# Kernel tuning notes

Hardware: AMD Instinct MI355X
Metric: run time of the kernel (lower is better)

The kernel has to match this reference:

```python
import jax, jax.numpy as jnp
import numpy as np

N = 100000
E = 1600000
IN, HID, OUT = 64, 128, 64
EPS = 1e-5


def _sage_conv(x, src, dst, w_l, b_l, w_r):
    # PyG SAGEConv (mean aggr): out = lin_l(mean_{j in N(i)} x_j) + lin_r(x_i)
    msgs = x[src]                                   # [E, d] gather
    agg = jax.ops.segment_sum(msgs, dst, num_segments=N)  # [N, d]
    deg = jax.ops.segment_sum(jnp.ones((E,), x.dtype), dst, num_segments=N)
    agg = agg / jnp.maximum(deg, 1.0)[:, None]      # mean over neighbors
    return agg @ w_l.T + b_l + x @ w_r.T


def _bn_eval(x, gamma, beta, mean, var):
    return (x - mean) * jax.lax.rsqrt(var + EPS) * gamma + beta


def setup_inputs() -> dict:
    key = jax.random.key(0)
    ks = jax.random.split(key, 16)
    x = jax.random.normal(ks[0], (N, IN), jnp.float32)
    edge_index = jax.random.randint(ks[1], (2, E), 0, N, jnp.int32)
    s1 = 1.0 / np.sqrt(IN)
    s2 = 1.0 / np.sqrt(HID)
    return {
        "x": x,
        "edge_index": edge_index,
        "w1l": jax.random.uniform(ks[2], (HID, IN), jnp.float32, -s1, s1),
        "b1l": jax.random.uniform(ks[3], (HID,), jnp.float32, -s1, s1),
        "w1r": jax.random.uniform(ks[4], (HID, IN), jnp.float32, -s1, s1),
        "bn1_gamma": jax.random.uniform(ks[5], (HID,), jnp.float32, 0.5, 1.5),
        "bn1_beta": jax.random.normal(ks[6], (HID,), jnp.float32) * 0.1,
        "bn1_mean": jax.random.normal(ks[7], (HID,), jnp.float32) * 0.1,
        "bn1_var": jax.random.uniform(ks[8], (HID,), jnp.float32, 0.5, 1.5),
        "w2l": jax.random.uniform(ks[9], (OUT, HID), jnp.float32, -s2, s2),
        "b2l": jax.random.uniform(ks[10], (OUT,), jnp.float32, -s2, s2),
        "w2r": jax.random.uniform(ks[11], (OUT, HID), jnp.float32, -s2, s2),
        "bn2_gamma": jax.random.uniform(ks[12], (OUT,), jnp.float32, 0.5, 1.5),
        "bn2_beta": jax.random.normal(ks[13], (OUT,), jnp.float32) * 0.1,
        "bn2_mean": jax.random.normal(ks[14], (OUT,), jnp.float32) * 0.1,
        "bn2_var": jax.random.uniform(ks[15], (OUT,), jnp.float32, 0.5, 1.5),
    }


def reference(x, edge_index, w1l, b1l, w1r, bn1_gamma, bn1_beta, bn1_mean, bn1_var,
              w2l, b2l, w2r, bn2_gamma, bn2_beta, bn2_mean, bn2_var):
    src, dst = edge_index[0], edge_index[1]
    # layer 1: SAGEConv -> BN -> ReLU (dropout is identity in eval mode)
    h = _sage_conv(x, src, dst, w1l, b1l, w1r)
    h = jax.nn.relu(_bn_eval(h, bn1_gamma, bn1_beta, bn1_mean, bn1_var))
    # layer 2: SAGEConv -> BN
    h = _sage_conv(h, src, dst, w2l, b2l, w2r)
    return _bn_eval(h, bn2_gamma, bn2_beta, bn2_mean, bn2_var)
```

## Files before the change

kernel.cpp:

```cpp
#include <hip/hip_runtime.h>

#define NN 100000
#define NE 1600000
#define EPSV 1e-5f

#define NBUK 196
#define TILE 2048
#define NTIL 782
#define CAP  9216

typedef __attribute__((ext_vector_type(8))) short bf16x8;
typedef __attribute__((ext_vector_type(4))) float f32x4;

__device__ inline unsigned short f2bf(float f) {
  unsigned u = __builtin_bit_cast(unsigned, f);
  unsigned r = u + 0x7FFFu + ((u >> 16) & 1u);
  return (unsigned short)(r >> 16);
}
__device__ inline float bf2f(unsigned short s) {
  unsigned u = ((unsigned)s) << 16;
  return __builtin_bit_cast(float, u);
}

__global__ __launch_bounds__(256) void k_bin(const int* __restrict__ src,
                                             const int* __restrict__ dst,
                                             int* __restrict__ gcur,
                                             unsigned* __restrict__ pairs) {
  __shared__ int cnt[NBUK];
  __shared__ int lo[NBUK];
  __shared__ int gbase[NBUK];
  __shared__ int ts[256];
  __shared__ unsigned stage[TILE];
  const int tid = threadIdx.x;
  const int e0 = blockIdx.x * TILE;
  const int m = min(TILE, NE - e0);

  for (int i = tid; i < NBUK; i += 256) cnt[i] = 0;
  __syncthreads();
  for (int i = tid; i < m; i += 256) {
    int d = dst[e0 + i];
    atomicAdd(&cnt[d >> 9], 1);
  }
  __syncthreads();
  int c = (tid < NBUK) ? cnt[tid] : 0;
  ts[tid] = c;
  __syncthreads();
  for (int d = 1; d < 256; d <<= 1) {
    int v = (tid >= d) ? ts[tid - d] : 0;
    __syncthreads();
    ts[tid] += v;
    __syncthreads();
  }
  if (tid < NBUK) {
    int ex = ts[tid] - c;
    lo[tid] = ex;
    gbase[tid] = atomicAdd(&gcur[tid], c);
    cnt[tid] = ex;
  }
  __syncthreads();
  for (int i = tid; i < m; i += 256) {
    int d = dst[e0 + i];
    int s = src[e0 + i];
    int b = d >> 9;
    int pos = atomicAdd(&cnt[b], 1);
    stage[pos] = ((unsigned)(d & 511) << 17) | (unsigned)s;
  }
  __syncthreads();
  for (int i = tid; i < m; i += 256) {
    int a = 0, z = NBUK - 1;
    while (a < z) {
      int mid = (a + z + 1) >> 1;
      if (lo[mid] <= i) a = mid; else z = mid - 1;
    }
    int rel = gbase[a] + (i - lo[a]);
    if (rel < CAP) pairs[(size_t)a * CAP + rel] = stage[i];
  }
}

__global__ __launch_bounds__(256) void k_bscan(const int* __restrict__ gcur,
                                               int* __restrict__ bucketBase) {
  __shared__ int ts[256];
  const int tid = threadIdx.x;
  int c = (tid < NBUK) ? min(gcur[tid], CAP) : 0;
  ts[tid] = c;
  __syncthreads();
  for (int d = 1; d < 256; d <<= 1) {
    int v = (tid >= d) ? ts[tid - d] : 0;
    __syncthreads();
    ts[tid] += v;
    __syncthreads();
  }
  if (tid < NBUK) bucketBase[tid] = ts[tid] - c;
}

__global__ __launch_bounds__(512) void k_build(const unsigned* __restrict__ pairs,
                                               const int* __restrict__ gcur,
                                               const int* __restrict__ bucketBase,
                                               int* __restrict__ deg,
                                               int* __restrict__ offset,
                                               int* __restrict__ csr) {
  __shared__ int hist[512];
  __shared__ int ts[512];
  __shared__ unsigned stage[CAP];
  const int tid = threadIdx.x;
  const int b = blockIdx.x;
  const int count = min(gcur[b], CAP);
  const int nbase = b * 512;
  const int nloc = min(512, NN - nbase);
  const unsigned* pb = pairs + (size_t)b * CAP;
  const int obase = bucketBase[b];

  hist[tid] = 0;
  __syncthreads();
  for (int i = tid; i < count; i += 512) {
    atomicAdd(&hist[pb[i] >> 17], 1);
  }
  __syncthreads();
  int s = hist[tid];
  ts[tid] = s;
  __syncthreads();
  for (int d = 1; d < 512; d <<= 1) {
    int v = (tid >= d) ? ts[tid - d] : 0;
    __syncthreads();
    ts[tid] += v;
    __syncthreads();
  }
  int ex = ts[tid] - s;
  if (tid < nloc) {
    deg[nbase + tid] = s;
    offset[nbase + tid] = obase + ex;
  }
  __syncthreads();
  hist[tid] = ex;
  __syncthreads();
  for (int i = tid; i < count; i += 512) {
    unsigned e = pb[i];
    int pos = atomicAdd(&hist[e >> 17], 1);
    stage[pos] = e & 0x1FFFFu;
  }
  __syncthreads();
  for (int i = tid; i < count; i += 512) csr[obase + i] = (int)stage[i];
}

__global__ __launch_bounds__(256) void k_wprep(const float* __restrict__ w1l,
                                               const float* __restrict__ w1r,
                                               const float* __restrict__ w2l,
                                               const float* __restrict__ w2r,
                                               const float* __restrict__ b1l,
                                               const float* __restrict__ g1,
                                               const float* __restrict__ be1,
                                               const float* __restrict__ m1,
                                               const float* __restrict__ v1,
                                               const float* __restrict__ b2l,
                                               const float* __restrict__ g2,
                                               const float* __restrict__ be2,
                                               const float* __restrict__ m2,
                                               const float* __restrict__ v2,
                                               unsigned short* __restrict__ w1c,
                                               unsigned short* __restrict__ w2c,
                                               float* __restrict__ bn) {
  int i = blockIdx.x * 256 + threadIdx.x;
  int o = i >> 7, k = i & 127;
  float vv1 = (k < 64) ? w1l[o * 64 + k] : w1r[o * 64 + (k - 64)];
  w1c[i] = f2bf(vv1);
  float vv2 = (o < 64) ? w2l[o * 128 + k] : w2r[(o - 64) * 128 + k];
  w2c[i] = f2bf(vv2);
  if (i < 128) {
    float sc = g1[i] * rsqrtf(v1[i] + EPSV);
    bn[i] = sc;
    bn[128 + i] = (b1l[i] - m1[i]) * sc + be1[i];
  }
  if (i < 64) {
    float sc = g2[i] * rsqrtf(v2[i] + EPSV);
    bn[256 + i] = sc;
    bn[320 + i] = (b2l[i] - m2[i]) * sc + be2[i];
  }
}

__global__ __launch_bounds__(256) void k_cvtx(const float* __restrict__ x,
                                              unsigned short* __restrict__ xb) {
  int i = blockIdx.x * 256 + threadIdx.x;
  float4 v = *(const float4*)(x + (size_t)i * 4);
  ushort4 o;
  o.x = f2bf(v.x); o.y = f2bf(v.y); o.z = f2bf(v.z); o.w = f2bf(v.w);
  *(ushort4*)(xb + (size_t)i * 4) = o;
}

__global__ __launch_bounds__(256) void k_aggregate(const unsigned short* __restrict__ xb,
                                                   const int* __restrict__ deg,
                                                   const int* __restrict__ offset,
                                                   const int* __restrict__ csr,
                                                   unsigned short* __restrict__ aggB) {
  int tid = threadIdx.x;
  int node = blockIdx.x * 32 + (tid >> 3);
  int j = tid & 7;
  int cnt = deg[node];
  const int* arow = csr + offset[node];
  float a0=0.f,a1=0.f,a2=0.f,a3=0.f,a4=0.f,a5=0.f,a6=0.f,a7=0.f;
  int k = 0;
  for (; k + 4 <= cnt; k += 4) {
    int s0 = arow[k], s1 = arow[k+1], s2 = arow[k+2], s3 = arow[k+3];
    uint4 v0 = *(const uint4*)(xb + (size_t)s0 * 64 + j * 8);
    uint4 v1 = *(const uint4*)(xb + (size_t)s1 * 64 + j * 8);
    uint4 v2 = *(const uint4*)(xb + (size_t)s2 * 64 + j * 8);
    uint4 v3 = *(const uint4*)(xb + (size_t)s3 * 64 + j * 8);
    a0 += bf2f(v0.x & 0xffff) + bf2f(v1.x & 0xffff) + bf2f(v2.x & 0xffff) + bf2f(v3.x & 0xffff);
    a1 += bf2f(v0.x >> 16)    + bf2f(v1.x >> 16)    + bf2f(v2.x >> 16)    + bf2f(v3.x >> 16);
    a2 += bf2f(v0.y & 0xffff) + bf2f(v1.y & 0xffff) + bf2f(v2.y & 0xffff) + bf2f(v3.y & 0xffff);
    a3 += bf2f(v0.y >> 16)    + bf2f(v1.y >> 16)    + bf2f(v2.y >> 16)    + bf2f(v3.y >> 16);
    a4 += bf2f(v0.z & 0xffff) + bf2f(v1.z & 0xffff) + bf2f(v2.z & 0xffff) + bf2f(v3.z & 0xffff);
    a5 += bf2f(v0.z >> 16)    + bf2f(v1.z >> 16)    + bf2f(v2.z >> 16)    + bf2f(v3.z >> 16);
    a6 += bf2f(v0.w & 0xffff) + bf2f(v1.w & 0xffff) + bf2f(v2.w & 0xffff) + bf2f(v3.w & 0xffff);
    a7 += bf2f(v0.w >> 16)    + bf2f(v1.w >> 16)    + bf2f(v2.w >> 16)    + bf2f(v3.w >> 16);
  }
  for (; k < cnt; ++k) {
    int s = arow[k];
    uint4 v = *(const uint4*)(xb + (size_t)s * 64 + j * 8);
    a0 += bf2f(v.x & 0xffff); a1 += bf2f(v.x >> 16);
    a2 += bf2f(v.y & 0xffff); a3 += bf2f(v.y >> 16);
    a4 += bf2f(v.z & 0xffff); a5 += bf2f(v.z >> 16);
    a6 += bf2f(v.w & 0xffff); a7 += bf2f(v.w >> 16);
  }
  float inv = 1.0f / fmaxf((float)cnt, 1.0f);
  ushort4 r0, r1;
  r0.x = f2bf(a0 * inv); r0.y = f2bf(a1 * inv); r0.z = f2bf(a2 * inv); r0.w = f2bf(a3 * inv);
  r1.x = f2bf(a4 * inv); r1.y = f2bf(a5 * inv); r1.z = f2bf(a6 * inv); r1.w = f2bf(a7 * inv);
  *(ushort4*)(aggB + (size_t)node * 64 + j * 8) = r0;
  *(ushort4*)(aggB + (size_t)node * 64 + j * 8 + 4) = r1;
}

__global__ __launch_bounds__(256) void k_gemm12(const unsigned short* __restrict__ aggB,
                                                const unsigned short* __restrict__ xb,
                                                const unsigned short* __restrict__ w1c,
                                                const unsigned short* __restrict__ w2c,
                                                const float* __restrict__ bn,
                                                unsigned short* __restrict__ t,
                                                unsigned short* __restrict__ r2) {
  __shared__ unsigned short wlds[32 * 512];
  __shared__ unsigned short hlds[4][2][16 * 128];
  __shared__ float bnlds[384];
  const int tid = threadIdx.x;
  const int w = tid >> 6;
  const int lane = tid & 63;
  const int lr = lane & 15;
  const int q = lane >> 4;
  const int base = blockIdx.x * 128 + w * 32;
  const int nA = base + lr, nB = base + 16 + lr;
  const int cA = min(nA, NN - 1), cB = min(nB, NN - 1);
  const int swz = (lr & 7) << 4;

  bf16x8 fA[4], fB[4];
  {
    const unsigned short* a = aggB + (size_t)cA * 64 + q * 8;
    const unsigned short* xx = xb + (size_t)cA * 64 + q * 8;
    fA[0] = *(const bf16x8*)a;        fA[1] = *(const bf16x8*)(a + 32);
    fA[2] = *(const bf16x8*)xx;       fA[3] = *(const bf16x8*)(xx + 32);
  }
  {
    const unsigned short* a = aggB + (size_t)cB * 64 + q * 8;
    const unsigned short* xx = xb + (size_t)cB * 64 + q * 8;
    fB[0] = *(const bf16x8*)a;        fB[1] = *(const bf16x8*)(a + 32);
    fB[2] = *(const bf16x8*)xx;       fB[3] = *(const bf16x8*)(xx + 32);
  }

  for (int i = tid; i < 384; i += 256) bnlds[i] = bn[i];
  for (int idx = tid; idx < 2048; idx += 256) {
    int f = idx >> 6, l = idx & 63;
    int gofs = ((f >> 2) * 16 + (l & 15)) * 128 + (f & 3) * 32 + (l >> 4) * 8;
    *(uint4*)&wlds[idx * 8] = *(const uint4*)&w1c[gofs];
  }
  __syncthreads();

  char* ldsA = (char*)&hlds[w][0][0];
  char* ldsB = (char*)&hlds[w][1][0];

#pragma unroll
  for (int ot = 0; ot < 8; ++ot) {
    const unsigned short* wp = &wlds[(ot * 4) * 512 + lane * 8];
    bf16x8 w0 = *(const bf16x8*)(wp);
    bf16x8 w1 = *(const bf16x8*)(wp + 512);
    bf16x8 w2 = *(const bf16x8*)(wp + 1024);
    bf16x8 w3 = *(const bf16x8*)(wp + 1536);
    f32x4 aA = {0.f, 0.f, 0.f, 0.f}, aB = {0.f, 0.f, 0.f, 0.f};
    aA = __builtin_amdgcn_mfma_f32_16x16x32_bf16(w0, fA[0], aA, 0, 0, 0);
    aA = __builtin_amdgcn_mfma_f32_16x16x32_bf16(w1, fA[1], aA, 0, 0, 0);
    aA = __builtin_amdgcn_mfma_f32_16x16x32_bf16(w2, fA[2], aA, 0, 0, 0);
    aA = __builtin_amdgcn_mfma_f32_16x16x32_bf16(w3, fA[3], aA, 0, 0, 0);
    aB = __builtin_amdgcn_mfma_f32_16x16x32_bf16(w0, fB[0], aB, 0, 0, 0);
    aB = __builtin_amdgcn_mfma_f32_16x16x32_bf16(w1, fB[1], aB, 0, 0, 0);
    aB = __builtin_amdgcn_mfma_f32_16x16x32_bf16(w2, fB[2], aB, 0, 0, 0);
    aB = __builtin_amdgcn_mfma_f32_16x16x32_bf16(w3, fB[3], aB, 0, 0, 0);
    const int o = ot * 16 + q * 4;
    float4 sc = *(const float4*)&bnlds[o];
    float4 sh = *(const float4*)&bnlds[128 + o];
    ushort4 hA, hB;
    hA.x = f2bf(fmaxf(aA[0] * sc.x + sh.x, 0.f));
    hA.y = f2bf(fmaxf(aA[1] * sc.y + sh.y, 0.f));
    hA.z = f2bf(fmaxf(aA[2] * sc.z + sh.z, 0.f));
    hA.w = f2bf(fmaxf(aA[3] * sc.w + sh.w, 0.f));
    hB.x = f2bf(fmaxf(aB[0] * sc.x + sh.x, 0.f));
    hB.y = f2bf(fmaxf(aB[1] * sc.y + sh.y, 0.f));
    hB.z = f2bf(fmaxf(aB[2] * sc.z + sh.z, 0.f));
    hB.w = f2bf(fmaxf(aB[3] * sc.w + sh.w, 0.f));
    const int wb = lr * 256 + ot * 32 + q * 8;
    *(ushort4*)(ldsA + (wb ^ swz)) = hA;
    *(ushort4*)(ldsB + (wb ^ swz)) = hB;
  }
  __syncthreads();

  for (int idx = tid; idx < 2048; idx += 256) {
    int f = idx >> 6, l = idx & 63;
    int gofs = ((f >> 2) * 16 + (l & 15)) * 128 + (f & 3) * 32 + (l >> 4) * 8;
    *(uint4*)&wlds[idx * 8] = *(const uint4*)&w2c[gofs];
  }
  __syncthreads();

  bf16x8 hA[4], hB[4];
#pragma unroll
  for (int jj = 0; jj < 4; ++jj) {
    const int rb = lr * 256 + jj * 64 + q * 16;
    hA[jj] = *(const bf16x8*)(ldsA + (rb ^ swz));
    hB[jj] = *(const bf16x8*)(ldsB + (rb ^ swz));
  }

#pragma unroll
  for (int ot = 0; ot < 8; ++ot) {
    const unsigned short* wp = &wlds[(ot * 4) * 512 + lane * 8];
    bf16x8 w0 = *(const bf16x8*)(wp);
    bf16x8 w1 = *(const bf16x8*)(wp + 512);
    bf16x8 w2 = *(const bf16x8*)(wp + 1024);
    bf16x8 w3 = *(const bf16x8*)(wp + 1536);
    f32x4 aA = {0.f, 0.f, 0.f, 0.f}, aB = {0.f, 0.f, 0.f, 0.f};
    aA = __builtin_amdgcn_mfma_f32_16x16x32_bf16(w0, hA[0], aA, 0, 0, 0);
    aA = __builtin_amdgcn_mfma_f32_16x16x32_bf16(w1, hA[1], aA, 0, 0, 0);
    aA = __builtin_amdgcn_mfma_f32_16x16x32_bf16(w2, hA[2], aA, 0, 0, 0);
    aA = __builtin_amdgcn_mfma_f32_16x16x32_bf16(w3, hA[3], aA, 0, 0, 0);
    aB = __builtin_amdgcn_mfma_f32_16x16x32_bf16(w0, hB[0], aB, 0, 0, 0);
    aB = __builtin_amdgcn_mfma_f32_16x16x32_bf16(w1, hB[1], aB, 0, 0, 0);
    aB = __builtin_amdgcn_mfma_f32_16x16x32_bf16(w2, hB[2], aB, 0, 0, 0);
    aB = __builtin_amdgcn_mfma_f32_16x16x32_bf16(w3, hB[3], aB, 0, 0, 0);
    ushort4 tv;
    if (ot < 4) {
      const int o = ot * 16 + q * 4;
      tv.x = f2bf(aA[0]); tv.y = f2bf(aA[1]); tv.z = f2bf(aA[2]); tv.w = f2bf(aA[3]);
      if (nA < NN) *(ushort4*)(t + (size_t)nA * 64 + o) = tv;
      tv.x = f2bf(aB[0]); tv.y = f2bf(aB[1]); tv.z = f2bf(aB[2]); tv.w = f2bf(aB[3]);
      if (nB < NN) *(ushort4*)(t + (size_t)nB * 64 + o) = tv;
    } else {
      const int o = (ot - 4) * 16 + q * 4;
      tv.x = f2bf(aA[0]); tv.y = f2bf(aA[1]); tv.z = f2bf(aA[2]); tv.w = f2bf(aA[3]);
      if (nA < NN) *(ushort4*)(r2 + (size_t)nA * 64 + o) = tv;
      tv.x = f2bf(aB[0]); tv.y = f2bf(aB[1]); tv.z = f2bf(aB[2]); tv.w = f2bf(aB[3]);
      if (nB < NN) *(ushort4*)(r2 + (size_t)nB * 64 + o) = tv;
    }
  }
}

__global__ __launch_bounds__(256) void k_agg2fin(const unsigned short* __restrict__ t,
                                                 const int* __restrict__ deg,
                                                 const int* __restrict__ offset,
                                                 const int* __restrict__ csr,
                                                 const unsigned short* __restrict__ r2,
                                                 const float* __restrict__ bn,
                                                 float* __restrict__ outp) {
  int tid = threadIdx.x;
  int node = blockIdx.x * 32 + (tid >> 3);
  int j = tid & 7;
  int cnt = deg[node];
  const int* arow = csr + offset[node];
  float a0=0.f,a1=0.f,a2=0.f,a3=0.f,a4=0.f,a5=0.f,a6=0.f,a7=0.f;
  int k = 0;
  for (; k + 4 <= cnt; k += 4) {
    int s0 = arow[k], s1 = arow[k+1], s2 = arow[k+2], s3 = arow[k+3];
    uint4 v0 = *(const uint4*)(t + (size_t)s0 * 64 + j * 8);
    uint4 v1 = *(const uint4*)(t + (size_t)s1 * 64 + j * 8);
    uint4 v2 = *(const uint4*)(t + (size_t)s2 * 64 + j * 8);
    uint4 v3 = *(const uint4*)(t + (size_t)s3 * 64 + j * 8);
    a0 += bf2f(v0.x & 0xffff) + bf2f(v1.x & 0xffff) + bf2f(v2.x & 0xffff) + bf2f(v3.x & 0xffff);
    a1 += bf2f(v0.x >> 16)    + bf2f(v1.x >> 16)    + bf2f(v2.x >> 16)    + bf2f(v3.x >> 16);
    a2 += bf2f(v0.y & 0xffff) + bf2f(v1.y & 0xffff) + bf2f(v2.y & 0xffff) + bf2f(v3.y & 0xffff);
    a3 += bf2f(v0.y >> 16)    + bf2f(v1.y >> 16)    + bf2f(v2.y >> 16)    + bf2f(v3.y >> 16);
    a4 += bf2f(v0.z & 0xffff) + bf2f(v1.z & 0xffff) + bf2f(v2.z & 0xffff) + bf2f(v3.z & 0xffff);
    a5 += bf2f(v0.z >> 16)    + bf2f(v1.z >> 16)    + bf2f(v2.z >> 16)    + bf2f(v3.z >> 16);
    a6 += bf2f(v0.w & 0xffff) + bf2f(v1.w & 0xffff) + bf2f(v2.w & 0xffff) + bf2f(v3.w & 0xffff);
    a7 += bf2f(v0.w >> 16)    + bf2f(v1.w >> 16)    + bf2f(v2.w >> 16)    + bf2f(v3.w >> 16);
  }
  for (; k < cnt; ++k) {
    int s = arow[k];
    uint4 v = *(const uint4*)(t + (size_t)s * 64 + j * 8);
    a0 += bf2f(v.x & 0xffff); a1 += bf2f(v.x >> 16);
    a2 += bf2f(v.y & 0xffff); a3 += bf2f(v.y >> 16);
    a4 += bf2f(v.z & 0xffff); a5 += bf2f(v.z >> 16);
    a6 += bf2f(v.w & 0xffff); a7 += bf2f(v.w >> 16);
  }
  float inv = 1.0f / fmaxf((float)cnt, 1.0f);
  int o = j * 8;
  uint4 rv = *(const uint4*)(r2 + (size_t)node * 64 + o);
  float r0 = bf2f(rv.x & 0xffff), r1 = bf2f(rv.x >> 16);
  float r2a = bf2f(rv.y & 0xffff), r3 = bf2f(rv.y >> 16);
  float r4 = bf2f(rv.z & 0xffff), r5 = bf2f(rv.z >> 16);
  float r6 = bf2f(rv.w & 0xffff), r7 = bf2f(rv.w >> 16);
  float4 sca = *(const float4*)(bn + 256 + o);
  float4 scb = *(const float4*)(bn + 256 + o + 4);
  float4 sha = *(const float4*)(bn + 320 + o);
  float4 shb = *(const float4*)(bn + 320 + o + 4);
  float4 o0, o1;
  o0.x = (a0 * inv + r0) * sca.x + sha.x;
  o0.y = (a1 * inv + r1) * sca.y + sha.y;
  o0.z = (a2 * inv + r2a) * sca.z + sha.z;
  o0.w = (a3 * inv + r3) * sca.w + sha.w;
  o1.x = (a4 * inv + r4) * scb.x + shb.x;
  o1.y = (a5 * inv + r5) * scb.y + shb.y;
  o1.z = (a6 * inv + r6) * scb.z + shb.z;
  o1.w = (a7 * inv + r7) * scb.w + shb.w;
  *(float4*)(outp + (size_t)node * 64 + o) = o0;
  *(float4*)(outp + (size_t)node * 64 + o + 4) = o1;
}

extern "C" void kernel_launch(void* const* d_in, const int* in_sizes, int n_in,
                              void* d_out, int out_size, void* d_ws, size_t ws_size,
                              hipStream_t stream) {
  const float* x   = (const float*)d_in[0];
  const int*   ei  = (const int*)d_in[1];
  const float* w1l = (const float*)d_in[2];
  const float* b1l = (const float*)d_in[3];
  const float* w1r = (const float*)d_in[4];
  const float* g1  = (const float*)d_in[5];
  const float* be1 = (const float*)d_in[6];
  const float* m1  = (const float*)d_in[7];
  const float* v1  = (const float*)d_in[8];
  const float* w2l = (const float*)d_in[9];
  const float* b2l = (const float*)d_in[10];
  const float* w2r = (const float*)d_in[11];
  const float* g2  = (const float*)d_in[12];
  const float* be2 = (const float*)d_in[13];
  const float* m2  = (const float*)d_in[14];
  const float* v2  = (const float*)d_in[15];
  float* outp = (float*)d_out;

  char* ws = (char*)d_ws;
  int*            gcur       = (int*)ws;
  int*            bucketBase = (int*)(ws + 1024);
  int*            deg        = (int*)(ws + 2048);
  int*            offset     = (int*)(ws + 402048);
  unsigned*       pairs      = (unsigned*)(ws + 802048);
  int*            csr        = (int*)(ws + 8027392);
  unsigned short* w1c        = (unsigned short*)(ws + 14427392);
  unsigned short* w2c        = (unsigned short*)(ws + 14460160);
  float*          bn         = (float*)(ws + 14492928);
  unsigned short* xb         = (unsigned short*)(ws + 14494976);
  unsigned short* aggB       = (unsigned short*)(ws + 27294976);
  unsigned short* t          = (unsigned short*)(ws + 40094976);
  unsigned short* r2         = (unsigned short*)(ws + 52894976);

  const int* srcp = ei;
  const int* dstp = ei + NE;

  hipMemsetAsync(gcur, 0, NBUK * sizeof(int), stream);
  hipLaunchKernelGGL(k_bin, dim3(NTIL), dim3(256), 0, stream,
                     srcp, dstp, gcur, pairs);
  hipLaunchKernelGGL(k_bscan, dim3(1), dim3(256), 0, stream, gcur, bucketBase);
  hipLaunchKernelGGL(k_build, dim3(NBUK), dim3(512), 0, stream,
                     pairs, gcur, bucketBase, deg, offset, csr);
  hipLaunchKernelGGL(k_wprep, dim3(64), dim3(256), 0, stream,
                     w1l, w1r, w2l, w2r, b1l, g1, be1, m1, v1,
                     b2l, g2, be2, m2, v2, w1c, w2c, bn);
  hipLaunchKernelGGL(k_cvtx, dim3(NN * 64 / 1024), dim3(256), 0, stream, x, xb);
  hipLaunchKernelGGL(k_aggregate, dim3(NN / 32), dim3(256), 0, stream,
                     xb, deg, offset, csr, aggB);
  hipLaunchKernelGGL(k_gemm12, dim3((NN + 127) / 128), dim3(256), 0, stream,
                     aggB, xb, w1c, w2c, bn, t, r2);
  hipLaunchKernelGGL(k_agg2fin, dim3(NN / 32), dim3(256), 0, stream,
                     t, deg, offset, csr, r2, bn, outp);
}
```

Before: 150.1 us.

## Fuse layer-1 neighbor aggregation into GEMM kernel and halve CSR bucket size

Removes the separate k_aggregate kernel. Each wave of the GEMM kernel now gathers and averages neighbor features for its 32 nodes and stages the bf16 means in LDS with an XOR swizzle, then feeds them straight to MFMA. This drops the aggB global round trip and one launch. The CSR build also switches to 256-node buckets (391 buckets, smaller capacity), which shortens the per-block scan and LDS staging but doubles the number of blocks in k_build. The halved CAP raises the chance of a bucket overflowing and silently dropping edges.

```diff
diff --git a/kernel.cpp b/kernel.cpp
--- a/kernel.cpp
+++ b/kernel.cpp
@@ -4,10 +4,10 @@
 #define NE 1600000
 #define EPSV 1e-5f
 
-#define NBUK 196
+#define NBUK 391
 #define TILE 2048
 #define NTIL 782
-#define CAP  9216
+#define CAP  4608
 
 typedef __attribute__((ext_vector_type(8))) short bf16x8;
 typedef __attribute__((ext_vector_type(4))) float f32x4;
@@ -39,11 +39,14 @@
   __syncthreads();
   for (int i = tid; i < m; i += 256) {
     int d = dst[e0 + i];
-    atomicAdd(&cnt[d >> 9], 1);
-  }
-  __syncthreads();
-  int c = (tid < NBUK) ? cnt[tid] : 0;
-  ts[tid] = c;
+    atomicAdd(&cnt[d >> 8], 1);
+  }
+  __syncthreads();
+  const int i0 = 2 * tid, i1 = 2 * tid + 1;
+  int c0 = (i0 < NBUK) ? cnt[i0] : 0;
+  int c1 = (i1 < NBUK) ? cnt[i1] : 0;
+  int s2 = c0 + c1;
+  ts[tid] = s2;
   __syncthreads();
   for (int d = 1; d < 256; d <<= 1) {
     int v = (tid >= d) ? ts[tid - d] : 0;
@@ -51,19 +54,19 @@
     ts[tid] += v;
     __syncthreads();
   }
-  if (tid < NBUK) {
-    int ex = ts[tid] - c;
-    lo[tid] = ex;
-    gbase[tid] = atomicAdd(&gcur[tid], c);
-    cnt[tid] = ex;
-  }
+  int ex = ts[tid] - s2;
+  if (i0 < NBUK) { lo[i0] = ex;      gbase[i0] = atomicAdd(&gcur[i0], c0); }
+  if (i1 < NBUK) { lo[i1] = ex + c0; gbase[i1] = atomicAdd(&gcur[i1], c1); }
+  __syncthreads();
+  if (i0 < NBUK) cnt[i0] = lo[i0];
+  if (i1 < NBUK) cnt[i1] = lo[i1];
   __syncthreads();
   for (int i = tid; i < m; i += 256) {
     int d = dst[e0 + i];
     int s = src[e0 + i];
-    int b = d >> 9;
+    int b = d >> 8;
     int pos = atomicAdd(&cnt[b], 1);
-    stage[pos] = ((unsigned)(d & 511) << 17) | (unsigned)s;
+    stage[pos] = ((unsigned)(d & 255) << 17) | (unsigned)s;
   }
   __syncthreads();
   for (int i = tid; i < m; i += 256) {
@@ -81,8 +84,11 @@
                                                int* __restrict__ bucketBase) {
   __shared__ int ts[256];
   const int tid = threadIdx.x;
-  int c = (tid < NBUK) ? min(gcur[tid], CAP) : 0;
-  ts[tid] = c;
+  const int i0 = 2 * tid, i1 = 2 * tid + 1;
+  int c0 = (i0 < NBUK) ? min(gcur[i0], CAP) : 0;
+  int c1 = (i1 < NBUK) ? min(gcur[i1], CAP) : 0;
+  int s2 = c0 + c1;
+  ts[tid] = s2;
   __syncthreads();
   for (int d = 1; d < 256; d <<= 1) {
     int v = (tid >= d) ? ts[tid - d] : 0;
@@ -90,7 +96,9 @@
     ts[tid] += v;
     __syncthreads();
   }
-  if (tid < NBUK) bucketBase[tid] = ts[tid] - c;
+  int ex = ts[tid] - s2;
+  if (i0 < NBUK) bucketBase[i0] = ex;
+  if (i1 < NBUK) bucketBase[i1] = ex + c0;
 }
 
 __global__ __launch_bounds__(512) void k_build(const unsigned* __restrict__ pairs,
@@ -99,39 +107,41 @@
                                                int* __restrict__ deg,
                                                int* __restrict__ offset,
                                                int* __restrict__ csr) {
-  __shared__ int hist[512];
-  __shared__ int ts[512];
+  __shared__ int hist[256];
+  __shared__ int ts[256];
   __shared__ unsigned stage[CAP];
   const int tid = threadIdx.x;
   const int b = blockIdx.x;
   const int count = min(gcur[b], CAP);
-  const int nbase = b * 512;
-  const int nloc = min(512, NN - nbase);
+  const int nbase = b * 256;
+  const int nloc = min(256, NN - nbase);
   const unsigned* pb = pairs + (size_t)b * CAP;
   const int obase = bucketBase[b];
 
-  hist[tid] = 0;
+  if (tid < 256) hist[tid] = 0;
   __syncthreads();
   for (int i = tid; i < count; i += 512) {
     atomicAdd(&hist[pb[i] >> 17], 1);
   }
   __syncthreads();
-  int s = hist[tid];
-  ts[tid] = s;
-  __syncthreads();
-  for (int d = 1; d < 512; d <<= 1) {
-    int v = (tid >= d) ? ts[tid - d] : 0;
-    __syncthreads();
-    ts[tid] += v;
-    __syncthreads();
-  }
-  int ex = ts[tid] - s;
-  if (tid < nloc) {
-    deg[nbase + tid] = s;
-    offset[nbase + tid] = obase + ex;
-  }
-  __syncthreads();
-  hist[tid] = ex;
+  int s = 0;
+  if (tid < 256) { s = hist[tid]; ts[tid] = s; }
+  __syncthreads();
+  for (int d = 1; d < 256; d <<= 1) {
+    int v = 0;
+    if (tid < 256 && tid >= d) v = ts[tid - d];
+    __syncthreads();
+    if (tid < 256) ts[tid] += v;
+    __syncthreads();
+  }
+  if (tid < 256) {
+    int ex = ts[tid] - s;
+    if (tid < nloc) {
+      deg[nbase + tid] = s;
+      offset[nbase + tid] = obase + ex;
+    }
+    hist[tid] = ex;
+  }
   __syncthreads();
   for (int i = tid; i < count; i += 512) {
     unsigned e = pb[i];
@@ -186,51 +196,10 @@
   *(ushort4*)(xb + (size_t)i * 4) = o;
 }
 
-__global__ __launch_bounds__(256) void k_aggregate(const unsigned short* __restrict__ xb,
-                                                   const int* __restrict__ deg,
-                                                   const int* __restrict__ offset,
-                                                   const int* __restrict__ csr,
-                                                   unsigned short* __restrict__ aggB) {
-  int tid = threadIdx.x;
-  int node = blockIdx.x * 32 + (tid >> 3);
-  int j = tid & 7;
-  int cnt = deg[node];
-  const int* arow = csr + offset[node];
-  float a0=0.f,a1=0.f,a2=0.f,a3=0.f,a4=0.f,a5=0.f,a6=0.f,a7=0.f;
-  int k = 0;
-  for (; k + 4 <= cnt; k += 4) {
-    int s0 = arow[k], s1 = arow[k+1], s2 = arow[k+2], s3 = arow[k+3];
-    uint4 v0 = *(const uint4*)(xb + (size_t)s0 * 64 + j * 8);
-    uint4 v1 = *(const uint4*)(xb + (size_t)s1 * 64 + j * 8);
-    uint4 v2 = *(const uint4*)(xb + (size_t)s2 * 64 + j * 8);
-    uint4 v3 = *(const uint4*)(xb + (size_t)s3 * 64 + j * 8);
-    a0 += bf2f(v0.x & 0xffff) + bf2f(v1.x & 0xffff) + bf2f(v2.x & 0xffff) + bf2f(v3.x & 0xffff);
-    a1 += bf2f(v0.x >> 16)    + bf2f(v1.x >> 16)    + bf2f(v2.x >> 16)    + bf2f(v3.x >> 16);
-    a2 += bf2f(v0.y & 0xffff) + bf2f(v1.y & 0xffff) + bf2f(v2.y & 0xffff) + bf2f(v3.y & 0xffff);
-    a3 += bf2f(v0.y >> 16)    + bf2f(v1.y >> 16)    + bf2f(v2.y >> 16)    + bf2f(v3.y >> 16);
-    a4 += bf2f(v0.z & 0xffff) + bf2f(v1.z & 0xffff) + bf2f(v2.z & 0xffff) + bf2f(v3.z & 0xffff);
-    a5 += bf2f(v0.z >> 16)    + bf2f(v1.z >> 16)    + bf2f(v2.z >> 16)    + bf2f(v3.z >> 16);
-    a6 += bf2f(v0.w & 0xffff) + bf2f(v1.w & 0xffff) + bf2f(v2.w & 0xffff) + bf2f(v3.w & 0xffff);
-    a7 += bf2f(v0.w >> 16)    + bf2f(v1.w >> 16)    + bf2f(v2.w >> 16)    + bf2f(v3.w >> 16);
-  }
-  for (; k < cnt; ++k) {
-    int s = arow[k];
-    uint4 v = *(const uint4*)(xb + (size_t)s * 64 + j * 8);
-    a0 += bf2f(v.x & 0xffff); a1 += bf2f(v.x >> 16);
-    a2 += bf2f(v.y & 0xffff); a3 += bf2f(v.y >> 16);
-    a4 += bf2f(v.z & 0xffff); a5 += bf2f(v.z >> 16);
-    a6 += bf2f(v.w & 0xffff); a7 += bf2f(v.w >> 16);
-  }
-  float inv = 1.0f / fmaxf((float)cnt, 1.0f);
-  ushort4 r0, r1;
-  r0.x = f2bf(a0 * inv); r0.y = f2bf(a1 * inv); r0.z = f2bf(a2 * inv); r0.w = f2bf(a3 * inv);
-  r1.x = f2bf(a4 * inv); r1.y = f2bf(a5 * inv); r1.z = f2bf(a6 * inv); r1.w = f2bf(a7 * inv);
-  *(ushort4*)(aggB + (size_t)node * 64 + j * 8) = r0;
-  *(ushort4*)(aggB + (size_t)node * 64 + j * 8 + 4) = r1;
-}
-
-__global__ __launch_bounds__(256) void k_gemm12(const unsigned short* __restrict__ aggB,
-                                                const unsigned short* __restrict__ xb,
+__global__ __launch_bounds__(256) void k_aggemm(const unsigned short* __restrict__ xb,
+                                                const int* __restrict__ deg,
+                                                const int* __restrict__ offset,
+                                                const int* __restrict__ csr,
                                                 const unsigned short* __restrict__ w1c,
                                                 const unsigned short* __restrict__ w2c,
                                                 const float* __restrict__ bn,
@@ -249,26 +218,66 @@
   const int cA = min(nA, NN - 1), cB = min(nB, NN - 1);
   const int swz = (lr & 7) << 4;
 
-  bf16x8 fA[4], fB[4];
-  {
-    const unsigned short* a = aggB + (size_t)cA * 64 + q * 8;
-    const unsigned short* xx = xb + (size_t)cA * 64 + q * 8;
-    fA[0] = *(const bf16x8*)a;        fA[1] = *(const bf16x8*)(a + 32);
-    fA[2] = *(const bf16x8*)xx;       fA[3] = *(const bf16x8*)(xx + 32);
-  }
-  {
-    const unsigned short* a = aggB + (size_t)cB * 64 + q * 8;
-    const unsigned short* xx = xb + (size_t)cB * 64 + q * 8;
-    fB[0] = *(const bf16x8*)a;        fB[1] = *(const bf16x8*)(a + 32);
-    fB[2] = *(const bf16x8*)xx;       fB[3] = *(const bf16x8*)(xx + 32);
-  }
-
   for (int i = tid; i < 384; i += 256) bnlds[i] = bn[i];
   for (int idx = tid; idx < 2048; idx += 256) {
     int f = idx >> 6, l = idx & 63;
     int gofs = ((f >> 2) * 16 + (l & 15)) * 128 + (f & 3) * 32 + (l >> 4) * 8;
     *(uint4*)&wlds[idx * 8] = *(const uint4*)&w1c[gofs];
   }
+
+  bf16x8 fA2, fA3, fB2, fB3;
+  fA2 = *(const bf16x8*)(xb + (size_t)cA * 64 + q * 8);
+  fA3 = *(const bf16x8*)(xb + (size_t)cA * 64 + q * 8 + 32);
+  fB2 = *(const bf16x8*)(xb + (size_t)cB * 64 + q * 8);
+  fB3 = *(const bf16x8*)(xb + (size_t)cB * 64 + q * 8 + 32);
+
+  char* astage = (char*)&hlds[w][0][0];
+  const int jj = lane & 7;
+  const int sub = lane >> 3;
+  for (int pass = 0; pass < 4; ++pass) {
+    const int nl = pass * 8 + sub;
+    const int cn = min(base + nl, NN - 1);
+    const int cnt = deg[cn];
+    const int* arow = csr + offset[cn];
+    float a0=0.f,a1=0.f,a2=0.f,a3=0.f,a4=0.f,a5=0.f,a6=0.f,a7=0.f;
+    int k = 0;
+    for (; k + 4 <= cnt; k += 4) {
+      int s0 = arow[k], s1 = arow[k+1], s2 = arow[k+2], s3 = arow[k+3];
+      uint4 v0 = *(const uint4*)(xb + (size_t)s0 * 64 + jj * 8);
+      uint4 v1 = *(const uint4*)(xb + (size_t)s1 * 64 + jj * 8);
+      uint4 v2 = *(const uint4*)(xb + (size_t)s2 * 64 + jj * 8);
+      uint4 v3 = *(const uint4*)(xb + (size_t)s3 * 64 + jj * 8);
+      a0 += bf2f(v0.x & 0xffff) + bf2f(v1.x & 0xffff) + bf2f(v2.x & 0xffff) + bf2f(v3.x & 0xffff);
+      a1 += bf2f(v0.x >> 16)    + bf2f(v1.x >> 16)    + bf2f(v2.x >> 16)    + bf2f(v3.x >> 16);
+      a2 += bf2f(v0.y & 0xffff) + bf2f(v1.y & 0xffff) + bf2f(v2.y & 0xffff) + bf2f(v3.y & 0xffff);
+      a3 += bf2f(v0.y >> 16)    + bf2f(v1.y >> 16)    + bf2f(v2.y >> 16)    + bf2f(v3.y >> 16);
+      a4 += bf2f(v0.z & 0xffff) + bf2f(v1.z & 0xffff) + bf2f(v2.z & 0xffff) + bf2f(v3.z & 0xffff);
+      a5 += bf2f(v0.z >> 16)    + bf2f(v1.z >> 16)    + bf2f(v2.z >> 16)    + bf2f(v3.z >> 16);
+      a6 += bf2f(v0.w & 0xffff) + bf2f(v1.w & 0xffff) + bf2f(v2.w & 0xffff) + bf2f(v3.w & 0xffff);
+      a7 += bf2f(v0.w >> 16)    + bf2f(v1.w >> 16)    + bf2f(v2.w >> 16)    + bf2f(v3.w >> 16);
+    }
+    for (; k < cnt; ++k) {
+      int s = arow[k];
+      uint4 v = *(const uint4*)(xb + (size_t)s * 64 + jj * 8);
+      a0 += bf2f(v.x & 0xffff); a1 += bf2f(v.x >> 16);
+      a2 += bf2f(v.y & 0xffff); a3 += bf2f(v.y >> 16);
+      a4 += bf2f(v.z & 0xffff); a5 += bf2f(v.z >> 16);
+      a6 += bf2f(v.w & 0xffff); a7 += bf2f(v.w >> 16);
+    }
+    float inv = 1.0f / fmaxf((float)cnt, 1.0f);
+    unsigned p0 = ((unsigned)f2bf(a1 * inv) << 16) | f2bf(a0 * inv);
+    unsigned p1 = ((unsigned)f2bf(a3 * inv) << 16) | f2bf(a2 * inv);
+    unsigned p2 = ((unsigned)f2bf(a5 * inv) << 16) | f2bf(a4 * inv);
+    unsigned p3 = ((unsigned)f2bf(a7 * inv) << 16) | f2bf(a6 * inv);
+    uint4 pk; pk.x = p0; pk.y = p1; pk.z = p2; pk.w = p3;
+    *(uint4*)(astage + nl * 128 + ((jj ^ (nl & 7)) << 4)) = pk;
+  }
+
+  const int slr = lr & 7;
+  bf16x8 fA0 = *(const bf16x8*)(astage + lr * 128 + ((q ^ slr) << 4));
+  bf16x8 fA1 = *(const bf16x8*)(astage + lr * 128 + (((q + 4) ^ slr) << 4));
+  bf16x8 fB0 = *(const bf16x8*)(astage + (16 + lr) * 128 + ((q ^ slr) << 4));
+  bf16x8 fB1 = *(const bf16x8*)(astage + (16 + lr) * 128 + (((q + 4) ^ slr) << 4));
   __syncthreads();
 
   char* ldsA = (char*)&hlds[w][0][0];
@@ -282,14 +291,14 @@
     bf16x8 w2 = *(const bf16x8*)(wp + 1024);
     bf16x8 w3 = *(const bf16x8*)(wp + 1536);
     f32x4 aA = {0.f, 0.f, 0.f, 0.f}, aB = {0.f, 0.f, 0.f, 0.f};
-    aA = __builtin_amdgcn_mfma_f32_16x16x32_bf16(w0, fA[0], aA, 0, 0, 0);
-    aA = __builtin_amdgcn_mfma_f32_16x16x32_bf16(w1, fA[1], aA, 0, 0, 0);
-    aA = __builtin_amdgcn_mfma_f32_16x16x32_bf16(w2, fA[2], aA, 0, 0, 0);
-    aA = __builtin_amdgcn_mfma_f32_16x16x32_bf16(w3, fA[3], aA, 0, 0, 0);
-    aB = __builtin_amdgcn_mfma_f32_16x16x32_bf16(w0, fB[0], aB, 0, 0, 0);
-    aB = __builtin_amdgcn_mfma_f32_16x16x32_bf16(w1, fB[1], aB, 0, 0, 0);
-    aB = __builtin_amdgcn_mfma_f32_16x16x32_bf16(w2, fB[2], aB, 0, 0, 0);
-    aB = __builtin_amdgcn_mfma_f32_16x16x32_bf16(w3, fB[3], aB, 0, 0, 0);
+    aA = __builtin_amdgcn_mfma_f32_16x16x32_bf16(w0, fA0, aA, 0, 0, 0);
+    aA = __builtin_amdgcn_mfma_f32_16x16x32_bf16(w1, fA1, aA, 0, 0, 0);
+    aA = __builtin_amdgcn_mfma_f32_16x16x32_bf16(w2, fA2, aA, 0, 0, 0);
+    aA = __builtin_amdgcn_mfma_f32_16x16x32_bf16(w3, fA3, aA, 0, 0, 0);
+    aB = __builtin_amdgcn_mfma_f32_16x16x32_bf16(w0, fB0, aB, 0, 0, 0);
+    aB = __builtin_amdgcn_mfma_f32_16x16x32_bf16(w1, fB1, aB, 0, 0, 0);
+    aB = __builtin_amdgcn_mfma_f32_16x16x32_bf16(w2, fB2, aB, 0, 0, 0);
+    aB = __builtin_amdgcn_mfma_f32_16x16x32_bf16(w3, fB3, aB, 0, 0, 0);
     const int o = ot * 16 + q * 4;
     float4 sc = *(const float4*)&bnlds[o];
     float4 sh = *(const float4*)&bnlds[128 + o];
@@ -317,10 +326,10 @@
 
   bf16x8 hA[4], hB[4];
 #pragma unroll
-  for (int jj = 0; jj < 4; ++jj) {
-    const int rb = lr * 256 + jj * 64 + q * 16;
-    hA[jj] = *(const bf16x8*)(ldsA + (rb ^ swz));
-    hB[jj] = *(const bf16x8*)(ldsB + (rb ^ swz));
+  for (int jx = 0; jx < 4; ++jx) {
+    const int rb = lr * 256 + jx * 64 + q * 16;
+    hA[jx] = *(const bf16x8*)(ldsA + (rb ^ swz));
+    hB[jx] = *(const bf16x8*)(ldsB + (rb ^ swz));
   }
 
 #pragma unroll
@@ -440,18 +449,17 @@
 
   char* ws = (char*)d_ws;
   int*            gcur       = (int*)ws;
-  int*            bucketBase = (int*)(ws + 1024);
-  int*            deg        = (int*)(ws + 2048);
-  int*            offset     = (int*)(ws + 402048);
-  unsigned*       pairs      = (unsigned*)(ws + 802048);
-  int*            csr        = (int*)(ws + 8027392);
-  unsigned short* w1c        = (unsigned short*)(ws + 14427392);
-  unsigned short* w2c        = (unsigned short*)(ws + 14460160);
-  float*          bn         = (float*)(ws + 14492928);
-  unsigned short* xb         = (unsigned short*)(ws + 14494976);
-  unsigned short* aggB       = (unsigned short*)(ws + 27294976);
-  unsigned short* t          = (unsigned short*)(ws + 40094976);
-  unsigned short* r2         = (unsigned short*)(ws + 52894976);
+  int*            bucketBase = (int*)(ws + 2048);
+  int*            deg        = (int*)(ws + 4096);
+  int*            offset     = (int*)(ws + 404096);
+  unsigned*       pairs      = (unsigned*)(ws + 804096);
+  int*            csr        = (int*)(ws + 8011008);
+  unsigned short* w1c        = (unsigned short*)(ws + 14411008);
+  unsigned short* w2c        = (unsigned short*)(ws + 14443776);
+  float*          bn         = (float*)(ws + 14476544);
+  unsigned short* xb         = (unsigned short*)(ws + 14478592);
+  unsigned short* t          = (unsigned short*)(ws + 27278592);
+  unsigned short* r2         = (unsigned short*)(ws + 40078592);
 
   const int* srcp = ei;
   const int* dstp = ei + NE;
@@ -466,10 +474,8 @@
                      w1l, w1r, w2l, w2r, b1l, g1, be1, m1, v1,
                      b2l, g2, be2, m2, v2, w1c, w2c, bn);
   hipLaunchKernelGGL(k_cvtx, dim3(NN * 64 / 1024), dim3(256), 0, stream, x, xb);
-  hipLaunchKernelGGL(k_aggregate, dim3(NN / 32), dim3(256), 0, stream,
-                     xb, deg, offset, csr, aggB);
-  hipLaunchKernelGGL(k_gemm12, dim3((NN + 127) / 128), dim3(256), 0, stream,
-                     aggB, xb, w1c, w2c, bn, t, r2);
+  hipLaunchKernelGGL(k_aggemm, dim3((NN + 127) / 128), dim3(256), 0, stream,
+                     xb, deg, offset, csr, w1c, w2c, bn, t, r2);
   hipLaunchKernelGGL(k_agg2fin, dim3(NN / 32), dim3(256), 0, stream,
                      t, deg, offset, csr, r2, bn, outp);
 }
```

Result: slower. 182.5 us (+21.6%).

## Replace atomic bucket scatter with per-tile counts, column scan, and gather in build

Applied to the files above, without the earlier changes.

The binning kernel now writes each tile's locally sorted edges contiguously and records per-tile bucket counts and offsets, instead of taking global atomic reservations and scattering into per-bucket regions. A new column-scan kernel computes each tile's offset within every bucket. The build kernel then gathers its bucket's edges from all tiles by binary search over those offsets. This removes global atomics and the memset, and makes the bucket order deterministic. It also fuses the weight-prep and x-conversion kernels into one launch. The cost is an extra kernel, scattered reads in the build kernel, and more shared memory per build block (two CAP-sized stages), which may lower occupancy.

```diff
diff --git a/kernel.cpp b/kernel.cpp
--- a/kernel.cpp
+++ b/kernel.cpp
@@ -24,22 +24,22 @@
 
 __global__ __launch_bounds__(256) void k_bin(const int* __restrict__ src,
                                              const int* __restrict__ dst,
-                                             int* __restrict__ gcur,
-                                             unsigned* __restrict__ pairs) {
+                                             unsigned* __restrict__ pairs,
+                                             int* __restrict__ tileCnt,
+                                             int* __restrict__ tileLo) {
   __shared__ int cnt[NBUK];
   __shared__ int lo[NBUK];
-  __shared__ int gbase[NBUK];
   __shared__ int ts[256];
   __shared__ unsigned stage[TILE];
   const int tid = threadIdx.x;
-  const int e0 = blockIdx.x * TILE;
+  const int t = blockIdx.x;
+  const int e0 = t * TILE;
   const int m = min(TILE, NE - e0);
 
   for (int i = tid; i < NBUK; i += 256) cnt[i] = 0;
   __syncthreads();
   for (int i = tid; i < m; i += 256) {
-    int d = dst[e0 + i];
-    atomicAdd(&cnt[d >> 9], 1);
+    atomicAdd(&cnt[dst[e0 + i] >> 9], 1);
   }
   __syncthreads();
   int c = (tid < NBUK) ? cnt[tid] : 0;
@@ -54,34 +54,60 @@
   if (tid < NBUK) {
     int ex = ts[tid] - c;
     lo[tid] = ex;
-    gbase[tid] = atomicAdd(&gcur[tid], c);
     cnt[tid] = ex;
   }
   __syncthreads();
   for (int i = tid; i < m; i += 256) {
     int d = dst[e0 + i];
     int s = src[e0 + i];
-    int b = d >> 9;
-    int pos = atomicAdd(&cnt[b], 1);
+    int pos = atomicAdd(&cnt[d >> 9], 1);
     stage[pos] = ((unsigned)(d & 511) << 17) | (unsigned)s;
   }
   __syncthreads();
-  for (int i = tid; i < m; i += 256) {
-    int a = 0, z = NBUK - 1;
-    while (a < z) {
-      int mid = (a + z + 1) >> 1;
-      if (lo[mid] <= i) a = mid; else z = mid - 1;
-    }
-    int rel = gbase[a] + (i - lo[a]);
-    if (rel < CAP) pairs[(size_t)a * CAP + rel] = stage[i];
-  }
-}
-
-__global__ __launch_bounds__(256) void k_bscan(const int* __restrict__ gcur,
+  for (int i = tid; i < m; i += 256) pairs[(size_t)t * TILE + i] = stage[i];
+  if (tid < NBUK) {
+    tileCnt[t * NBUK + tid] = cnt[tid] - lo[tid];
+    tileLo[t * NBUK + tid] = lo[tid];
+  }
+}
+
+__global__ __launch_bounds__(256) void k_colscan(const int* __restrict__ tileCnt,
+                                                 int* __restrict__ colBase,
+                                                 int* __restrict__ total) {
+  __shared__ int ts[256];
+  const int tid = threadIdx.x;
+  const int b = blockIdx.x;
+  int v[4];
+  int s = 0;
+#pragma unroll
+  for (int j = 0; j < 4; ++j) {
+    int tt = tid * 4 + j;
+    v[j] = (tt < NTIL) ? tileCnt[tt * NBUK + b] : 0;
+    s += v[j];
+  }
+  ts[tid] = s;
+  __syncthreads();
+  for (int d = 1; d < 256; d <<= 1) {
+    int x = (tid >= d) ? ts[tid - d] : 0;
+    __syncthreads();
+    ts[tid] += x;
+    __syncthreads();
+  }
+  int run = ts[tid] - s;
+#pragma unroll
+  for (int j = 0; j < 4; ++j) {
+    int tt = tid * 4 + j;
+    if (tt < NTIL) colBase[(size_t)b * NTIL + tt] = run;
+    run += v[j];
+  }
+  if (tid == 255) total[b] = ts[255];
+}
+
+__global__ __launch_bounds__(256) void k_bscan(const int* __restrict__ total,
                                                int* __restrict__ bucketBase) {
   __shared__ int ts[256];
   const int tid = threadIdx.x;
-  int c = (tid < NBUK) ? min(gcur[tid], CAP) : 0;
+  int c = (tid < NBUK) ? min(total[tid], CAP) : 0;
   ts[tid] = c;
   __syncthreads();
   for (int d = 1; d < 256; d <<= 1) {
@@ -94,26 +120,43 @@
 }
 
 __global__ __launch_bounds__(512) void k_build(const unsigned* __restrict__ pairs,
-                                               const int* __restrict__ gcur,
+                                               const int* __restrict__ tileLo,
+                                               const int* __restrict__ colBase,
+                                               const int* __restrict__ total,
                                                const int* __restrict__ bucketBase,
                                                int* __restrict__ deg,
                                                int* __restrict__ offset,
                                                int* __restrict__ csr) {
+  __shared__ unsigned stageA[CAP];
+  __shared__ unsigned stageB[CAP];
+  __shared__ int colB[NTIL];
+  __shared__ int tLo[NTIL];
   __shared__ int hist[512];
   __shared__ int ts[512];
-  __shared__ unsigned stage[CAP];
   const int tid = threadIdx.x;
   const int b = blockIdx.x;
-  const int count = min(gcur[b], CAP);
+  const int count = min(total[b], CAP);
   const int nbase = b * 512;
   const int nloc = min(512, NN - nbase);
-  const unsigned* pb = pairs + (size_t)b * CAP;
   const int obase = bucketBase[b];
 
+  for (int i = tid; i < NTIL; i += 512) {
+    colB[i] = colBase[(size_t)b * NTIL + i];
+    tLo[i] = tileLo[i * NBUK + b];
+  }
   hist[tid] = 0;
   __syncthreads();
   for (int i = tid; i < count; i += 512) {
-    atomicAdd(&hist[pb[i] >> 17], 1);
+    int a = 0, z = NTIL - 1;
+    while (a < z) {
+      int mid = (a + z + 1) >> 1;
+      if (colB[mid] <= i) a = mid; else z = mid - 1;
+    }
+    stageA[i] = pairs[(size_t)a * TILE + tLo[a] + (i - colB[a])];
+  }
+  __syncthreads();
+  for (int i = tid; i < count; i += 512) {
+    atomicAdd(&hist[stageA[i] >> 17], 1);
   }
   __syncthreads();
   int s = hist[tid];
@@ -130,60 +173,59 @@
     deg[nbase + tid] = s;
     offset[nbase + tid] = obase + ex;
   }
-  __syncthreads();
   hist[tid] = ex;
   __syncthreads();
   for (int i = tid; i < count; i += 512) {
-    unsigned e = pb[i];
+    unsigned e = stageA[i];
     int pos = atomicAdd(&hist[e >> 17], 1);
-    stage[pos] = e & 0x1FFFFu;
-  }
-  __syncthreads();
-  for (int i = tid; i < count; i += 512) csr[obase + i] = (int)stage[i];
-}
-
-__global__ __launch_bounds__(256) void k_wprep(const float* __restrict__ w1l,
-                                               const float* __restrict__ w1r,
-                                               const float* __restrict__ w2l,
-                                               const float* __restrict__ w2r,
-                                               const float* __restrict__ b1l,
-                                               const float* __restrict__ g1,
-                                               const float* __restrict__ be1,
-                                               const float* __restrict__ m1,
-                                               const float* __restrict__ v1,
-                                               const float* __restrict__ b2l,
-                                               const float* __restrict__ g2,
-                                               const float* __restrict__ be2,
-                                               const float* __restrict__ m2,
-                                               const float* __restrict__ v2,
-                                               unsigned short* __restrict__ w1c,
-                                               unsigned short* __restrict__ w2c,
-                                               float* __restrict__ bn) {
-  int i = blockIdx.x * 256 + threadIdx.x;
-  int o = i >> 7, k = i & 127;
-  float vv1 = (k < 64) ? w1l[o * 64 + k] : w1r[o * 64 + (k - 64)];
-  w1c[i] = f2bf(vv1);
-  float vv2 = (o < 64) ? w2l[o * 128 + k] : w2r[(o - 64) * 128 + k];
-  w2c[i] = f2bf(vv2);
-  if (i < 128) {
-    float sc = g1[i] * rsqrtf(v1[i] + EPSV);
-    bn[i] = sc;
-    bn[128 + i] = (b1l[i] - m1[i]) * sc + be1[i];
-  }
-  if (i < 64) {
-    float sc = g2[i] * rsqrtf(v2[i] + EPSV);
-    bn[256 + i] = sc;
-    bn[320 + i] = (b2l[i] - m2[i]) * sc + be2[i];
-  }
-}
-
-__global__ __launch_bounds__(256) void k_cvtx(const float* __restrict__ x,
-                                              unsigned short* __restrict__ xb) {
-  int i = blockIdx.x * 256 + threadIdx.x;
-  float4 v = *(const float4*)(x + (size_t)i * 4);
+    stageB[pos] = e & 0x1FFFFu;
+  }
+  __syncthreads();
+  for (int i = tid; i < count; i += 512) csr[obase + i] = (int)stageB[i];
+}
+
+__global__ __launch_bounds__(256) void k_prep(const float* __restrict__ x,
+                                              unsigned short* __restrict__ xb,
+                                              const float* __restrict__ w1l,
+                                              const float* __restrict__ w1r,
+                                              const float* __restrict__ w2l,
+                                              const float* __restrict__ w2r,
+                                              const float* __restrict__ b1l,
+                                              const float* __restrict__ g1,
+                                              const float* __restrict__ be1,
+                                              const float* __restrict__ m1,
+                                              const float* __restrict__ v1,
+                                              const float* __restrict__ b2l,
+                                              const float* __restrict__ g2,
+                                              const float* __restrict__ be2,
+                                              const float* __restrict__ m2,
+                                              const float* __restrict__ v2,
+                                              unsigned short* __restrict__ w1c,
+                                              unsigned short* __restrict__ w2c,
+                                              float* __restrict__ bn) {
+  int gi = blockIdx.x * 256 + threadIdx.x;
+  float4 v = *(const float4*)(x + (size_t)gi * 4);
   ushort4 o;
   o.x = f2bf(v.x); o.y = f2bf(v.y); o.z = f2bf(v.z); o.w = f2bf(v.w);
-  *(ushort4*)(xb + (size_t)i * 4) = o;
+  *(ushort4*)(xb + (size_t)gi * 4) = o;
+  if (blockIdx.x < 64) {
+    int i = gi;
+    int oo = i >> 7, k = i & 127;
+    float vv1 = (k < 64) ? w1l[oo * 64 + k] : w1r[oo * 64 + (k - 64)];
+    w1c[i] = f2bf(vv1);
+    float vv2 = (oo < 64) ? w2l[oo * 128 + k] : w2r[(oo - 64) * 128 + k];
+    w2c[i] = f2bf(vv2);
+    if (i < 128) {
+      float sc = g1[i] * rsqrtf(v1[i] + EPSV);
+      bn[i] = sc;
+      bn[128 + i] = (b1l[i] - m1[i]) * sc + be1[i];
+    }
+    if (i < 64) {
+      float sc = g2[i] * rsqrtf(v2[i] + EPSV);
+      bn[256 + i] = sc;
+      bn[320 + i] = (b2l[i] - m2[i]) * sc + be2[i];
+    }
+  }
 }
 
 __global__ __launch_bounds__(256) void k_aggregate(const unsigned short* __restrict__ xb,
@@ -439,33 +481,36 @@
   float* outp = (float*)d_out;
 
   char* ws = (char*)d_ws;
-  int*            gcur       = (int*)ws;
-  int*            bucketBase = (int*)(ws + 1024);
-  int*            deg        = (int*)(ws + 2048);
-  int*            offset     = (int*)(ws + 402048);
-  unsigned*       pairs      = (unsigned*)(ws + 802048);
-  int*            csr        = (int*)(ws + 8027392);
-  unsigned short* w1c        = (unsigned short*)(ws + 14427392);
-  unsigned short* w2c        = (unsigned short*)(ws + 14460160);
-  float*          bn         = (float*)(ws + 14492928);
-  unsigned short* xb         = (unsigned short*)(ws + 14494976);
-  unsigned short* aggB       = (unsigned short*)(ws + 27294976);
-  unsigned short* t          = (unsigned short*)(ws + 40094976);
-  unsigned short* r2         = (unsigned short*)(ws + 52894976);
+  int*            tileCnt    = (int*)ws;
+  int*            tileLo     = (int*)(ws + 613120);
+  int*            colBase    = (int*)(ws + 1226240);
+  int*            total      = (int*)(ws + 1839360);
+  int*            bucketBase = (int*)(ws + 1840384);
+  int*            deg        = (int*)(ws + 1841408);
+  int*            offset     = (int*)(ws + 2241408);
+  unsigned*       pairs      = (unsigned*)(ws + 2641408);
+  int*            csr        = (int*)(ws + 9047552);
+  unsigned short* w1c        = (unsigned short*)(ws + 15447552);
+  unsigned short* w2c        = (unsigned short*)(ws + 15480320);
+  float*          bn         = (float*)(ws + 15513088);
+  unsigned short* xb         = (unsigned short*)(ws + 15515136);
+  unsigned short* aggB       = (unsigned short*)(ws + 28315136);
+  unsigned short* t          = (unsigned short*)(ws + 41115136);
+  unsigned short* r2         = (unsigned short*)(ws + 53915136);
 
   const int* srcp = ei;
   const int* dstp = ei + NE;
 
-  hipMemsetAsync(gcur, 0, NBUK * sizeof(int), stream);
+  hipLaunchKernelGGL(k_prep, dim3(NN * 64 / 1024), dim3(256), 0, stream,
+                     x, xb, w1l, w1r, w2l, w2r, b1l, g1, be1, m1, v1,
+                     b2l, g2, be2, m2, v2, w1c, w2c, bn);
   hipLaunchKernelGGL(k_bin, dim3(NTIL), dim3(256), 0, stream,
-                     srcp, dstp, gcur, pairs);
-  hipLaunchKernelGGL(k_bscan, dim3(1), dim3(256), 0, stream, gcur, bucketBase);
+                     srcp, dstp, pairs, tileCnt, tileLo);
+  hipLaunchKernelGGL(k_colscan, dim3(NBUK), dim3(256), 0, stream,
+                     tileCnt, colBase, total);
+  hipLaunchKernelGGL(k_bscan, dim3(1), dim3(256), 0, stream, total, bucketBase);
   hipLaunchKernelGGL(k_build, dim3(NBUK), dim3(512), 0, stream,
-                     pairs, gcur, bucketBase, deg, offset, csr);
-  hipLaunchKernelGGL(k_wprep, dim3(64), dim3(256), 0, stream,
-                     w1l, w1r, w2l, w2r, b1l, g1, be1, m1, v1,
-                     b2l, g2, be2, m2, v2, w1c, w2c, bn);
-  hipLaunchKernelGGL(k_cvtx, dim3(NN * 64 / 1024), dim3(256), 0, stream, x, xb);
+                     pairs, tileLo, colBase, total, bucketBase, deg, offset, csr);
   hipLaunchKernelGGL(k_aggregate, dim3(NN / 32), dim3(256), 0, stream,
                      xb, deg, offset, csr, aggB);
   hipLaunchKernelGGL(k_gemm12, dim3((NN + 127) / 128), dim3(256), 0, stream,
```

New measurement: 140.4 us. -6.4%, faster.
